# Kernel optimization log

Hardware: AMD Instinct MI355X
Metric: run time of the kernel (lower is better)

Reference implementation:

```python
import jax, jax.numpy as jnp
import numpy as np
import math

B, N, D, H = 4, 1024, 256, 8  # batch, points, dim_V, heads
DH = D // H                   # per-head dim = 32
INF = jnp.float32(1e38)


def setup_inputs() -> dict:
    key = jax.random.key(0)
    ks = jax.random.split(key, 16)
    s = 0.02
    inp = {
        "X_lift": jax.random.normal(ks[0], (B, N, 3), jnp.float32),
        "Y_lift": jax.random.normal(ks[1], (B, N, D), jnp.float32),
        "X_pairs": jax.random.normal(ks[2], (B, N, N, 3), jnp.float32),
        "presence_q": (jax.random.uniform(ks[3], (B, N)) < 0.9).astype(jnp.float32),
        "presence_k": (jax.random.uniform(ks[4], (B, N)) < 0.9).astype(jnp.float32),
        # projection weights, stored [in, out]
        "Wq": jax.random.normal(ks[5], (D, D), jnp.float32) * s,
        "bq": jnp.zeros((D,), jnp.float32),
        "Wk": jax.random.normal(ks[6], (D, D), jnp.float32) * s,
        "bk": jnp.zeros((D,), jnp.float32),
        "Wv": jax.random.normal(ks[7], (D, D), jnp.float32) * s,
        "bv": jnp.zeros((D,), jnp.float32),
        "Wo": jax.random.normal(ks[8], (D, D), jnp.float32) * s,
        "bo": jnp.zeros((D,), jnp.float32),
        # per-head location-bias MLPs: Linear(3,3) -> ReLU -> Linear(3,1)
        "Wg1": jax.random.normal(ks[9], (H, 3, 3), jnp.float32) * 0.5,
        "bg1": jnp.zeros((H, 3), jnp.float32),
        "wg2": jax.random.normal(ks[10], (H, 3), jnp.float32) * 0.5,
        "bg2": jnp.zeros((H,), jnp.float32),
    }
    return inp


def reference(X_lift, Y_lift, X_pairs, presence_q, presence_k,
              Wq, bq, Wk, bk, Wv, bv, Wo, bo, Wg1, bg1, wg2, bg2):
    # X_lift is unused by the original forward (keys=queries=values=Y_lift)
    Q = Y_lift @ Wq + bq          # [B,N,D]
    K = Y_lift @ Wk + bk
    V = Y_lift @ Wv + bv

    # split into heads, head-major layout [H,B,N,DH]
    Qh = Q.reshape(B, N, H, DH).transpose(2, 0, 1, 3)
    Kh = K.reshape(B, N, H, DH).transpose(2, 0, 1, 3)
    Vh = V.reshape(B, N, H, DH).transpose(2, 0, 1, 3)

    content = jnp.einsum('hbnd,hbmd->hbnm', Qh, Kh) / math.sqrt(D)

    # per-head pairwise location bias MLP on X_pairs [B,N,N,3]
    hid = jax.nn.relu(jnp.einsum('bnmc,hcd->hbnmd', X_pairs, Wg1)
                      + bg1[:, None, None, None, :])       # [H,B,N,N,3]
    loc = jnp.einsum('hbnmd,hd->hbnm', hid, wg2) + bg2[:, None, None, None]

    logits = content + loc                                  # [H,B,N,N]

    pq = presence_q[None, :, :, None]                       # [1,B,N,1]
    logits = pq * logits - (1.0 - pq) * INF
    pk = presence_k[None, :, None, :]                       # [1,B,1,N]
    logits = pk * logits - (1.0 - pk) * INF

    A = jax.nn.softmax(logits, axis=-1)                     # [H,B,N,N]
    Oh = jnp.einsum('hbnm,hbmd->hbnd', A, Vh)               # [H,B,N,DH]
    O = V + Oh.transpose(1, 2, 0, 3).reshape(B, N, D)       # residual on values
    O = O + jax.nn.relu(O @ Wo + bo)
    return O
```

## Files before the change

### kernel.cpp

```cpp
#include <hip/hip_runtime.h>
#include <hip/hip_bf16.h>
#include <math.h>

typedef __bf16 bf16;
typedef __bf16 bf16x4 __attribute__((ext_vector_type(4)));
typedef __bf16 bf16x8 __attribute__((ext_vector_type(8)));
typedef float f32x2 __attribute__((ext_vector_type(2)));
typedef float f32x4 __attribute__((ext_vector_type(4)));

#define NB 4
#define NN 1024
#define ND 256
#define NH 8
#define INFV 1e38f
#define RTHR2 11.5f
#define LOG2E 1.44269504f
#define ZSPLIT 4

__device__ __forceinline__ f32x4 mfma16(bf16x8 a, bf16x8 b, f32x4 c) {
    return __builtin_amdgcn_mfma_f32_16x16x32_bf16(a, b, c, 0, 0, 0);
}
__device__ __forceinline__ f32x2 sp2(float v) { return f32x2{v, v}; }
__device__ __forceinline__ f32x2 fma2(f32x2 a, float b, f32x2 c) {
    return __builtin_elementwise_fma(a, sp2(b), c);
}

template<int MODE>
__global__ __launch_bounds__(256)
void gemm_k(const float* __restrict__ A,
            const float* __restrict__ W0, const float* __restrict__ b0,
            const float* __restrict__ W1, const float* __restrict__ b1,
            const float* __restrict__ W2, const float* __restrict__ b2,
            float* __restrict__ Fo2, bf16* __restrict__ G0,
            bf16* __restrict__ G1, bf16* __restrict__ Gt,
            float* __restrict__ Fo1, const float* __restrict__ addsrc)
{
    const int z = blockIdx.z;
    const float* W    = (z == 0) ? W0 : (z == 1) ? W1 : W2;
    const float* bias = (z == 0) ? b0 : (z == 1) ? b1 : b2;

    const int brow = blockIdx.x * 64;
    const int bcol = blockIdx.y * 64;
    const int t    = threadIdx.x;
    const int lane = t & 63;
    const int w    = t >> 6;
    const int wr   = w >> 1, wc = w & 1;
    const int g    = lane >> 4;
    const int l16  = lane & 15;

    __shared__ bf16 As[64][40];
    __shared__ bf16 Wt[64][40];

    f32x4 acc[2][2];
    #pragma unroll
    for (int i = 0; i < 2; ++i)
        #pragma unroll
        for (int j = 0; j < 2; ++j) acc[i][j] = f32x4{0.f, 0.f, 0.f, 0.f};

    const int ar = t >> 2, aj = (t & 3) * 8;
    const int wcid = t & 63, wk = (t >> 6) * 8;

    for (int k0 = 0; k0 < 256; k0 += 32) {
        {
            const float4 v0 = *(const float4*)&A[(size_t)(brow + ar)*ND + k0 + aj];
            const float4 v1 = *(const float4*)&A[(size_t)(brow + ar)*ND + k0 + aj + 4];
            bf16x8 w8 = { (bf16)v0.x, (bf16)v0.y, (bf16)v0.z, (bf16)v0.w,
                          (bf16)v1.x, (bf16)v1.y, (bf16)v1.z, (bf16)v1.w };
            *(bf16x8*)&As[ar][aj] = w8;
        }
        {
            bf16x8 w8;
            #pragma unroll
            for (int p = 0; p < 8; ++p)
                w8[p] = (bf16)W[(size_t)(k0 + wk + p)*ND + bcol + wcid];
            *(bf16x8*)&Wt[wcid][wk] = w8;
        }
        __syncthreads();

        bf16x8 af[2], bfj[2];
        #pragma unroll
        for (int i = 0; i < 2; ++i) af[i]  = *(const bf16x8*)&As[wr*32 + i*16 + l16][8*g];
        #pragma unroll
        for (int j = 0; j < 2; ++j) bfj[j] = *(const bf16x8*)&Wt[wc*32 + j*16 + l16][8*g];
        #pragma unroll
        for (int j = 0; j < 2; ++j)
            #pragma unroll
            for (int i = 0; i < 2; ++i) acc[i][j] = mfma16(af[i], bfj[j], acc[i][j]);
        __syncthreads();
    }

    #pragma unroll
    for (int j = 0; j < 2; ++j) {
        const int col = bcol + wc*32 + j*16 + l16;
        const float bj = bias[col];
        #pragma unroll
        for (int i = 0; i < 2; ++i) {
            const int row0 = brow + wr*32 + i*16 + 4*g;
            if (MODE == 1) {
                #pragma unroll
                for (int r = 0; r < 4; ++r) {
                    const size_t idx = (size_t)(row0 + r)*ND + col;
                    Fo1[idx] = addsrc[idx] + fmaxf(acc[i][j][r] + bj, 0.f);
                }
            } else if (z < 2) {
                bf16* Go = (z == 0) ? G0 : G1;
                #pragma unroll
                for (int r = 0; r < 4; ++r)
                    Go[(size_t)(row0 + r)*ND + col] = (bf16)(acc[i][j][r] + bj);
            } else {
                float vv[4];
                #pragma unroll
                for (int r = 0; r < 4; ++r) {
                    vv[r] = acc[i][j][r] + bj;
                    Fo2[(size_t)(row0 + r)*ND + col] = vv[r];
                }
                const int b2 = row0 >> 10;
                const int n0 = row0 & 1023;
                bf16x4 tv = { (bf16)vv[0], (bf16)vv[1], (bf16)vv[2], (bf16)vv[3] };
                *(bf16x4*)&Gt[((size_t)b2*ND + col)*NN + n0] = tv;
            }
        }
    }
}

__global__ __launch_bounds__(512, 4)
void attn_k(const bf16* __restrict__ Qb, const bf16* __restrict__ Kb,
            const bf16* __restrict__ Vt, const float* __restrict__ Xpg,
            const float* __restrict__ prq, const float* __restrict__ prk,
            const float* __restrict__ Wg1, const float* __restrict__ bg1,
            const float* __restrict__ wg2, const float* __restrict__ bg2,
            float* __restrict__ Ohp, float* __restrict__ ml)
{
    const int b    = blockIdx.y;
    const int q0   = blockIdx.x * 16;
    const int z    = blockIdx.z;
    const int mb0  = z * (NN/ZSPLIT);
    const int t    = threadIdx.x;
    const int w    = t >> 6;
    const int lane = t & 63;
    const int g    = lane >> 4;
    const int l16  = lane & 15;
    const int NT   = NN/ZSPLIT/32;

    __shared__ float Xps[2][16*132];
    __shared__ bf16  Ps[8][16][40];

    float g1[3][3], gb1[3], g2v[3], gb2v;
    #pragma unroll
    for (int c = 0; c < 3; ++c)
        #pragma unroll
        for (int d = 0; d < 3; ++d) g1[c][d] = Wg1[(w*3 + c)*3 + d];
    #pragma unroll
    for (int d = 0; d < 3; ++d) { gb1[d] = bg1[w*3 + d]; g2v[d] = wg2[w*3 + d]*LOG2E; }
    gb2v = bg2[w]*LOG2E;
    const float sscale = 0.0625f * LOG2E;

    const bf16x8 qf = *(const bf16x8*)&Qb[((size_t)b*NN + q0 + l16)*ND + w*32 + 8*g];

    bool okq[4];
    #pragma unroll
    for (int r = 0; r < 4; ++r)
        okq[r] = prq[b*NN + q0 + 4*g + r] > 0.5f;

    float m_run[4], l_run[4];
    f32x4 oh[2];
    #pragma unroll
    for (int r = 0; r < 4; ++r) { m_run[r] = -INFINITY; l_run[r] = 0.f; }
    oh[0] = f32x4{0.f,0.f,0.f,0.f};
    oh[1] = f32x4{0.f,0.f,0.f,0.f};

    const bf16*  kp0 = &Kb[((size_t)b*NN + mb0 + l16)*ND + w*32 + 8*g];
    const bf16*  kp1 = kp0 + (size_t)16*ND;
    const bf16*  vp0 = &Vt[((size_t)b*ND + w*32 + l16)*NN + mb0 + 8*g];
    const bf16*  vp1 = vp0 + (size_t)16*NN;
    const int    xq  = t >> 5, xm = t & 31;
    const float* xpp = &Xpg[(((size_t)b*NN + q0 + xq)*NN + mb0 + xm)*3];
    const float* pkp = &prk[(size_t)b*NN + mb0 + l16];

    bf16x8 kf0 = *(const bf16x8*)kp0;
    bf16x8 kf1 = *(const bf16x8*)kp1;
    bf16x8 vf0 = *(const bf16x8*)vp0;
    bf16x8 vf1 = *(const bf16x8*)vp1;
    float  xx = xpp[0], xy = xpp[1], xz = xpp[2];
    float  pk0 = pkp[0], pk1 = pkp[16];
    {
        float* dst = &Xps[0][xq*132 + xm*4];
        dst[0] = xx; dst[1] = xy; dst[2] = xz;
    }
    __syncthreads();

    for (int it = 0; it < NT; ++it) {
        const int cur = it & 1;

        bf16x8 kn0, kn1, vn0, vn1;
        float  xnx, xny, xnz, pn0, pn1;
        if (it + 1 < NT) {
            const int off = (it + 1) * 32;
            kn0 = *(const bf16x8*)(kp0 + (size_t)off*ND);
            kn1 = *(const bf16x8*)(kp1 + (size_t)off*ND);
            vn0 = *(const bf16x8*)(vp0 + off);
            vn1 = *(const bf16x8*)(vp1 + off);
            xnx = xpp[(size_t)off*3];
            xny = xpp[(size_t)off*3 + 1];
            xnz = xpp[(size_t)off*3 + 2];
            pn0 = pkp[off]; pn1 = pkp[off + 16];
        }

        const f32x4 zero = {0.f,0.f,0.f,0.f};
        f32x4 s[2];
        s[0] = mfma16(qf, kf0, zero);
        s[1] = mfma16(qf, kf1, zero);

        const bool okk0 = pk0 > 0.5f;
        const bool okk1 = pk1 > 0.5f;

        float lv[2][4];
        #pragma unroll
        for (int mg = 0; mg < 2; ++mg) {
            const bool okkm = mg ? okk1 : okk0;
            const int m = mg*16 + l16;
            #pragma unroll
            for (int rp = 0; rp < 2; ++rp) {
                const int q = 4*g + 2*rp;
                const float4 xa = *(const float4*)&Xps[cur][q*132 + m*4];
                const float4 xb = *(const float4*)&Xps[cur][(q+1)*132 + m*4];
                const f32x2 vx = {xa.x, xb.x};
                const f32x2 vy = {xa.y, xb.y};
                const f32x2 vz = {xa.z, xb.z};
                f32x2 h0 = fma2(vz, g1[2][0], fma2(vy, g1[1][0], fma2(vx, g1[0][0], sp2(gb1[0]))));
                f32x2 h1 = fma2(vz, g1[2][1], fma2(vy, g1[1][1], fma2(vx, g1[0][1], sp2(gb1[1]))));
                f32x2 h2 = fma2(vz, g1[2][2], fma2(vy, g1[1][2], fma2(vx, g1[0][2], sp2(gb1[2]))));
                const f32x2 zz = {0.f, 0.f};
                h0 = __builtin_elementwise_max(h0, zz);
                h1 = __builtin_elementwise_max(h1, zz);
                h2 = __builtin_elementwise_max(h2, zz);
                f32x2 loc = fma2(h2, g2v[2], fma2(h1, g2v[1], fma2(h0, g2v[0], sp2(gb2v))));
                const f32x2 s2 = { s[mg][2*rp], s[mg][2*rp+1] };
                const f32x2 y = fma2(s2, sscale, loc);
                lv[mg][2*rp]   = (okq[2*rp]   && okkm) ? y.x : -INFV;
                lv[mg][2*rp+1] = (okq[2*rp+1] && okkm) ? y.y : -INFV;
            }
        }

        float pm[4];
        #pragma unroll
        for (int r = 0; r < 4; ++r) pm[r] = fmaxf(lv[0][r], lv[1][r]);
        const bool cond = (pm[0] <= m_run[0] + RTHR2) && (pm[1] <= m_run[1] + RTHR2)
                       && (pm[2] <= m_run[2] + RTHR2) && (pm[3] <= m_run[3] + RTHR2);
        if (!__all((int)cond)) {
            #pragma unroll
            for (int r = 0; r < 4; ++r) {
                float mx = pm[r];
                mx = fmaxf(mx, __shfl_xor(mx, 1));
                mx = fmaxf(mx, __shfl_xor(mx, 2));
                mx = fmaxf(mx, __shfl_xor(mx, 4));
                mx = fmaxf(mx, __shfl_xor(mx, 8));
                const float mnew = fmaxf(m_run[r], mx);
                const float corr = exp2f(m_run[r] - mnew);
                l_run[r] *= corr;
                oh[0][r] *= corr;
                oh[1][r] *= corr;
                m_run[r] = mnew;
            }
        }
        #pragma unroll
        for (int r = 0; r < 4; ++r) {
            const float p0 = exp2f(lv[0][r] - m_run[r]);
            const float p1 = exp2f(lv[1][r] - m_run[r]);
            Ps[w][4*g + r][l16]      = (bf16)p0;
            Ps[w][4*g + r][16 + l16] = (bf16)p1;
            l_run[r] += p0 + p1;
        }

        asm volatile("s_waitcnt lgkmcnt(0)" ::: "memory");
        __builtin_amdgcn_sched_barrier(0);

        const bf16x8 pf = *(const bf16x8*)&Ps[w][l16][8*g];
        oh[0] = mfma16(pf, vf0, oh[0]);
        oh[1] = mfma16(pf, vf1, oh[1]);

        if (it + 1 < NT) {
            float* dst = &Xps[cur ^ 1][xq*132 + xm*4];
            dst[0] = xnx; dst[1] = xny; dst[2] = xnz;
            kf0 = kn0; kf1 = kn1; vf0 = vn0; vf1 = vn1;
            pk0 = pn0; pk1 = pn1;
        }
        __syncthreads();
    }

    #pragma unroll
    for (int r = 0; r < 4; ++r) {
        float ls = l_run[r];
        ls += __shfl_xor(ls, 1);
        ls += __shfl_xor(ls, 2);
        ls += __shfl_xor(ls, 4);
        ls += __shfl_xor(ls, 8);
        const int n = q0 + 4*g + r;
        #pragma unroll
        for (int dg = 0; dg < 2; ++dg) {
            const int col = w*32 + dg*16 + l16;
            Ohp[(((size_t)z*NB + b)*NN + n)*ND + col] = oh[dg][r];
        }
        if (l16 == 0) {
            const size_t mi = ((((size_t)z*NB + b)*NN + n)*NH + w)*2;
            ml[mi]   = m_run[r];
            ml[mi+1] = ls;
        }
    }
}

__global__ __launch_bounds__(256)
void comb_k(const float* __restrict__ Ohp, const float* __restrict__ ml,
            const float* __restrict__ Vf, float* __restrict__ O1)
{
    const int idx = blockIdx.x * 256 + threadIdx.x;
    const int dq = idx & 63;
    const int bn = idx >> 6;
    const int d0 = dq * 4;
    const int h  = dq >> 3;

    const size_t base = ((size_t)bn*NH + h)*2;
    const size_t zstr = (size_t)NB*NN*NH*2;
    float mz[ZSPLIT], lz[ZSPLIT];
    float M = -INFINITY;
    #pragma unroll
    for (int zi = 0; zi < ZSPLIT; ++zi) {
        mz[zi] = ml[base + zi*zstr];
        lz[zi] = ml[base + zi*zstr + 1];
        M = fmaxf(M, mz[zi]);
    }
    float wz[ZSPLIT], den = 0.f;
    #pragma unroll
    for (int zi = 0; zi < ZSPLIT; ++zi) {
        wz[zi] = exp2f(mz[zi] - M);
        den = fmaf(lz[zi], wz[zi], den);
    }
    const float inv = 1.f / den;

    const size_t e = (size_t)bn*ND + d0;
    f32x4 num = {0.f,0.f,0.f,0.f};
    #pragma unroll
    for (int zi = 0; zi < ZSPLIT; ++zi) {
        const f32x4 o = *(const f32x4*)&Ohp[e + (size_t)zi*NB*NN*ND];
        #pragma unroll
        for (int r = 0; r < 4; ++r) num[r] = fmaf(o[r], wz[zi], num[r]);
    }
    const f32x4 vf = *(const f32x4*)&Vf[e];
    f32x4 out;
    #pragma unroll
    for (int r = 0; r < 4; ++r) out[r] = vf[r] + num[r]*inv;
    *(f32x4*)&O1[e] = out;
}

extern "C" void kernel_launch(void* const* d_in, const int* in_sizes, int n_in,
                              void* d_out, int out_size, void* d_ws, size_t ws_size,
                              hipStream_t stream)
{
    const float* Y   = (const float*)d_in[1];
    const float* Xp  = (const float*)d_in[2];
    const float* prq = (const float*)d_in[3];
    const float* prk = (const float*)d_in[4];
    const float* Wq  = (const float*)d_in[5];
    const float* bq  = (const float*)d_in[6];
    const float* Wk  = (const float*)d_in[7];
    const float* bk  = (const float*)d_in[8];
    const float* Wv  = (const float*)d_in[9];
    const float* bv  = (const float*)d_in[10];
    const float* Wo  = (const float*)d_in[11];
    const float* bo  = (const float*)d_in[12];
    const float* Wg1 = (const float*)d_in[13];
    const float* bg1 = (const float*)d_in[14];
    const float* wg2 = (const float*)d_in[15];
    const float* bg2 = (const float*)d_in[16];
    float* out = (float*)d_out;

    const size_t BND = (size_t)NB * NN * ND;
    float* Vf  = (float*)d_ws;
    float* Ohp = Vf + BND;
    float* ml  = Ohp + (size_t)ZSPLIT*BND;
    bf16*  Qb  = (bf16*)(ml + (size_t)ZSPLIT*NB*NN*NH*2);
    bf16*  Kb  = Qb + BND;
    bf16*  Vt  = Kb + BND;
    float* O1  = (float*)Qb;

    gemm_k<0><<<dim3(64, 4, 3), 256, 0, stream>>>(
        Y, Wq, bq, Wk, bk, Wv, bv,
        Vf, Qb, Kb, Vt, nullptr, nullptr);

    attn_k<<<dim3(NN/16, NB, ZSPLIT), 512, 0, stream>>>(
        Qb, Kb, Vt, Xp, prq, prk, Wg1, bg1, wg2, bg2, Ohp, ml);

    comb_k<<<dim3(1024), 256, 0, stream>>>(Ohp, ml, Vf, O1);

    gemm_k<1><<<dim3(64, 4, 1), 256, 0, stream>>>(
        O1, Wo, bo, Wo, bo, Wo, bo,
        nullptr, nullptr, nullptr, nullptr, out, O1);
}
```

Baseline: 72.62 us.

## Transpose attention MFMA layout so P stays in registers via ds_bpermute

The score and PV MFMAs now take their operands in swapped order, so each lane owns a single query row. This lets the running max and sum become scalars, and P is repacked to bf16 with v_cvt_pk_bf16_f32 and redistributed with ds_bpermute instead of a round trip through the shared-memory Ps buffer. The V and key-presence loads move into the current iteration rather than being prefetched, the Xps stores become float4 writes, and the loop is unrolled by two. This aims to cut LDS traffic and the per-row reductions, at the cost of exposing V load latency and adding bpermute/select instructions.

```diff
diff --git a/kernel.cpp b/kernel.cpp
--- a/kernel.cpp
+++ b/kernel.cpp
@@ -23,6 +23,11 @@
 __device__ __forceinline__ f32x2 sp2(float v) { return f32x2{v, v}; }
 __device__ __forceinline__ f32x2 fma2(f32x2 a, float b, f32x2 c) {
     return __builtin_elementwise_fma(a, sp2(b), c);
+}
+__device__ __forceinline__ unsigned cvtpk(float lo, float hi) {
+    unsigned r;
+    asm("v_cvt_pk_bf16_f32 %0, %1, %2" : "=v"(r) : "v"(lo), "v"(hi));
+    return r;
 }
 
 template<int MODE>
@@ -143,7 +148,6 @@
     const int NT   = NN/ZSPLIT/32;
 
     __shared__ float Xps[2][16*132];
-    __shared__ bf16  Ps[8][16][40];
 
     float g1[3][3], gb1[3], g2v[3], gb2v;
     #pragma unroll
@@ -156,18 +160,15 @@
     const float sscale = 0.0625f * LOG2E;
 
     const bf16x8 qf = *(const bf16x8*)&Qb[((size_t)b*NN + q0 + l16)*ND + w*32 + 8*g];
-
-    bool okq[4];
-    #pragma unroll
-    for (int r = 0; r < 4; ++r)
-        okq[r] = prq[b*NN + q0 + 4*g + r] > 0.5f;
-
-    float m_run[4], l_run[4];
+    const bool okq = prq[b*NN + q0 + l16] > 0.5f;
+
+    float m_run = -INFINITY, l_run = 0.f;
     f32x4 oh[2];
-    #pragma unroll
-    for (int r = 0; r < 4; ++r) { m_run[r] = -INFINITY; l_run[r] = 0.f; }
     oh[0] = f32x4{0.f,0.f,0.f,0.f};
     oh[1] = f32x4{0.f,0.f,0.f,0.f};
+
+    const int aA = (((g & 1) * 2) * 16 + l16) * 4;
+    const int aB = aA + 64;
 
     const bf16*  kp0 = &Kb[((size_t)b*NN + mb0 + l16)*ND + w*32 + 8*g];
     const bf16*  kp1 = kp0 + (size_t)16*ND;
@@ -175,55 +176,50 @@
     const bf16*  vp1 = vp0 + (size_t)16*NN;
     const int    xq  = t >> 5, xm = t & 31;
     const float* xpp = &Xpg[(((size_t)b*NN + q0 + xq)*NN + mb0 + xm)*3];
-    const float* pkp = &prk[(size_t)b*NN + mb0 + l16];
+    const float* pkp = &prk[(size_t)b*NN + mb0];
 
     bf16x8 kf0 = *(const bf16x8*)kp0;
     bf16x8 kf1 = *(const bf16x8*)kp1;
-    bf16x8 vf0 = *(const bf16x8*)vp0;
-    bf16x8 vf1 = *(const bf16x8*)vp1;
-    float  xx = xpp[0], xy = xpp[1], xz = xpp[2];
-    float  pk0 = pkp[0], pk1 = pkp[16];
     {
-        float* dst = &Xps[0][xq*132 + xm*4];
-        dst[0] = xx; dst[1] = xy; dst[2] = xz;
+        float4 xv = { xpp[0], xpp[1], xpp[2], 0.f };
+        *(float4*)&Xps[0][xq*132 + xm*4] = xv;
     }
     __syncthreads();
 
+    #pragma unroll 2
     for (int it = 0; it < NT; ++it) {
         const int cur = it & 1;
-
-        bf16x8 kn0, kn1, vn0, vn1;
-        float  xnx, xny, xnz, pn0, pn1;
+        const int m0  = it * 32;
+
+        const bf16x8 vf0 = *(const bf16x8*)(vp0 + m0);
+        const bf16x8 vf1 = *(const bf16x8*)(vp1 + m0);
+        const float4 pka = *(const float4*)&pkp[m0 + 4*g];
+        const float4 pkb = *(const float4*)&pkp[m0 + 16 + 4*g];
+        bf16x8 kn0, kn1;
+        float  xnx = 0.f, xny = 0.f, xnz = 0.f;
         if (it + 1 < NT) {
             const int off = (it + 1) * 32;
             kn0 = *(const bf16x8*)(kp0 + (size_t)off*ND);
             kn1 = *(const bf16x8*)(kp1 + (size_t)off*ND);
-            vn0 = *(const bf16x8*)(vp0 + off);
-            vn1 = *(const bf16x8*)(vp1 + off);
             xnx = xpp[(size_t)off*3];
             xny = xpp[(size_t)off*3 + 1];
             xnz = xpp[(size_t)off*3 + 2];
-            pn0 = pkp[off]; pn1 = pkp[off + 16];
         }
 
         const f32x4 zero = {0.f,0.f,0.f,0.f};
         f32x4 s[2];
-        s[0] = mfma16(qf, kf0, zero);
-        s[1] = mfma16(qf, kf1, zero);
-
-        const bool okk0 = pk0 > 0.5f;
-        const bool okk1 = pk1 > 0.5f;
+        s[0] = mfma16(kf0, qf, zero);
+        s[1] = mfma16(kf1, qf, zero);
 
         float lv[2][4];
         #pragma unroll
         for (int mg = 0; mg < 2; ++mg) {
-            const bool okkm = mg ? okk1 : okk0;
-            const int m = mg*16 + l16;
+            const float4 pk4 = mg ? pkb : pka;
             #pragma unroll
             for (int rp = 0; rp < 2; ++rp) {
-                const int q = 4*g + 2*rp;
-                const float4 xa = *(const float4*)&Xps[cur][q*132 + m*4];
-                const float4 xb = *(const float4*)&Xps[cur][(q+1)*132 + m*4];
+                const int mA = mg*16 + 4*g + 2*rp;
+                const float4 xa = *(const float4*)&Xps[cur][l16*132 + mA*4];
+                const float4 xb = *(const float4*)&Xps[cur][l16*132 + (mA+1)*4];
                 const f32x2 vx = {xa.x, xb.x};
                 const f32x2 vy = {xa.y, xb.y};
                 const f32x2 vz = {xa.z, xb.z};
@@ -237,75 +233,74 @@
                 f32x2 loc = fma2(h2, g2v[2], fma2(h1, g2v[1], fma2(h0, g2v[0], sp2(gb2v))));
                 const f32x2 s2 = { s[mg][2*rp], s[mg][2*rp+1] };
                 const f32x2 y = fma2(s2, sscale, loc);
-                lv[mg][2*rp]   = (okq[2*rp]   && okkm) ? y.x : -INFV;
-                lv[mg][2*rp+1] = (okq[2*rp+1] && okkm) ? y.y : -INFV;
+                lv[mg][2*rp]   = (okq && pk4[2*rp]   > 0.5f) ? y.x : -INFV;
+                lv[mg][2*rp+1] = (okq && pk4[2*rp+1] > 0.5f) ? y.y : -INFV;
             }
         }
 
-        float pm[4];
-        #pragma unroll
-        for (int r = 0; r < 4; ++r) pm[r] = fmaxf(lv[0][r], lv[1][r]);
-        const bool cond = (pm[0] <= m_run[0] + RTHR2) && (pm[1] <= m_run[1] + RTHR2)
-                       && (pm[2] <= m_run[2] + RTHR2) && (pm[3] <= m_run[3] + RTHR2);
-        if (!__all((int)cond)) {
+        float pm = fmaxf(fmaxf(fmaxf(lv[0][0], lv[0][1]), fmaxf(lv[0][2], lv[0][3])),
+                         fmaxf(fmaxf(lv[1][0], lv[1][1]), fmaxf(lv[1][2], lv[1][3])));
+        if (!__all((int)(pm <= m_run + RTHR2))) {
+            float mx = pm;
+            mx = fmaxf(mx, __shfl_xor(mx, 16));
+            mx = fmaxf(mx, __shfl_xor(mx, 32));
+            const float mnew = fmaxf(m_run, mx);
+            const float corr = exp2f(m_run - mnew);
+            l_run *= corr;
             #pragma unroll
-            for (int r = 0; r < 4; ++r) {
-                float mx = pm[r];
-                mx = fmaxf(mx, __shfl_xor(mx, 1));
-                mx = fmaxf(mx, __shfl_xor(mx, 2));
-                mx = fmaxf(mx, __shfl_xor(mx, 4));
-                mx = fmaxf(mx, __shfl_xor(mx, 8));
-                const float mnew = fmaxf(m_run[r], mx);
-                const float corr = exp2f(m_run[r] - mnew);
-                l_run[r] *= corr;
-                oh[0][r] *= corr;
-                oh[1][r] *= corr;
-                m_run[r] = mnew;
-            }
-        }
+            for (int r = 0; r < 4; ++r) { oh[0][r] *= corr; oh[1][r] *= corr; }
+            m_run = mnew;
+        }
+        float pp0[4], pp1[4];
         #pragma unroll
         for (int r = 0; r < 4; ++r) {
-            const float p0 = exp2f(lv[0][r] - m_run[r]);
-            const float p1 = exp2f(lv[1][r] - m_run[r]);
-            Ps[w][4*g + r][l16]      = (bf16)p0;
-            Ps[w][4*g + r][16 + l16] = (bf16)p1;
-            l_run[r] += p0 + p1;
-        }
-
-        asm volatile("s_waitcnt lgkmcnt(0)" ::: "memory");
-        __builtin_amdgcn_sched_barrier(0);
-
-        const bf16x8 pf = *(const bf16x8*)&Ps[w][l16][8*g];
-        oh[0] = mfma16(pf, vf0, oh[0]);
-        oh[1] = mfma16(pf, vf1, oh[1]);
+            pp0[r] = exp2f(lv[0][r] - m_run);
+            pp1[r] = exp2f(lv[1][r] - m_run);
+        }
+        l_run += (pp0[0] + pp0[1]) + (pp0[2] + pp0[3])
+               + (pp1[0] + pp1[1]) + (pp1[2] + pp1[3]);
+
+        const unsigned A0 = cvtpk(pp0[0], pp0[1]);
+        const unsigned A1 = cvtpk(pp0[2], pp0[3]);
+        const unsigned B0 = cvtpk(pp1[0], pp1[1]);
+        const unsigned B1 = cvtpk(pp1[2], pp1[3]);
+        const bool lo = (lane < 32);
+        const int w0a = __builtin_amdgcn_ds_bpermute(aA, (int)A0);
+        const int w0b = __builtin_amdgcn_ds_bpermute(aA, (int)B0);
+        const int w1a = __builtin_amdgcn_ds_bpermute(aA, (int)A1);
+        const int w1b = __builtin_amdgcn_ds_bpermute(aA, (int)B1);
+        const int w2a = __builtin_amdgcn_ds_bpermute(aB, (int)A0);
+        const int w2b = __builtin_amdgcn_ds_bpermute(aB, (int)B0);
+        const int w3a = __builtin_amdgcn_ds_bpermute(aB, (int)A1);
+        const int w3b = __builtin_amdgcn_ds_bpermute(aB, (int)B1);
+        union { int i[4]; bf16x8 v; } pu;
+        pu.i[0] = lo ? w0a : w0b;
+        pu.i[1] = lo ? w1a : w1b;
+        pu.i[2] = lo ? w2a : w2b;
+        pu.i[3] = lo ? w3a : w3b;
+
+        oh[0] = mfma16(vf0, pu.v, oh[0]);
+        oh[1] = mfma16(vf1, pu.v, oh[1]);
 
         if (it + 1 < NT) {
-            float* dst = &Xps[cur ^ 1][xq*132 + xm*4];
-            dst[0] = xnx; dst[1] = xny; dst[2] = xnz;
-            kf0 = kn0; kf1 = kn1; vf0 = vn0; vf1 = vn1;
-            pk0 = pn0; pk1 = pn1;
+            float4 xv = { xnx, xny, xnz, 0.f };
+            *(float4*)&Xps[cur ^ 1][xq*132 + xm*4] = xv;
+            kf0 = kn0; kf1 = kn1;
         }
         __syncthreads();
     }
 
-    #pragma unroll
-    for (int r = 0; r < 4; ++r) {
-        float ls = l_run[r];
-        ls += __shfl_xor(ls, 1);
-        ls += __shfl_xor(ls, 2);
-        ls += __shfl_xor(ls, 4);
-        ls += __shfl_xor(ls, 8);
-        const int n = q0 + 4*g + r;
-        #pragma unroll
-        for (int dg = 0; dg < 2; ++dg) {
-            const int col = w*32 + dg*16 + l16;
-            Ohp[(((size_t)z*NB + b)*NN + n)*ND + col] = oh[dg][r];
-        }
-        if (l16 == 0) {
-            const size_t mi = ((((size_t)z*NB + b)*NN + n)*NH + w)*2;
-            ml[mi]   = m_run[r];
-            ml[mi+1] = ls;
-        }
+    float ls = l_run;
+    ls += __shfl_xor(ls, 16);
+    ls += __shfl_xor(ls, 32);
+    const int n = q0 + l16;
+    const size_t obase = (((size_t)z*NB + b)*NN + n)*ND + w*32;
+    *(f32x4*)&Ohp[obase + 4*g]      = oh[0];
+    *(f32x4*)&Ohp[obase + 16 + 4*g] = oh[1];
+    if (g == 0) {
+        const size_t mi = ((((size_t)z*NB + b)*NN + n)*NH + w)*2;
+        ml[mi]   = m_run;
+        ml[mi+1] = ls;
     }
 }
 
```

After: 77.29 us. 1.06x slower.
